# Optimization experiments

Measured on AMD Instinct MI355X. Metric: run time of the kernel, lower is better.

Reference implementation:

```python
import jax, jax.numpy as jnp
import numpy as np

EPS = 1e-05


def setup_inputs() -> dict:
    key = jax.random.key(0)
    k1, k2 = jax.random.split(key)
    shape = (4, 1, 192, 192, 192)  # [B, C=1, D, H, W]
    y_pred = jax.random.normal(k1, shape, dtype=jnp.float32)
    y_true = jax.random.normal(k2, shape, dtype=jnp.float32)
    return {"y_pred": y_pred, "y_true": y_true}


def reference(y_pred, y_true):
    # ones-filter conv is exactly a global sum over channel+spatial dims.
    Ii, Ji = y_true, y_pred
    axes = tuple(range(1, Ii.ndim))  # sum over C, D, H, W -> per-batch scalar
    win_size = jnp.asarray(np.prod(Ii.shape[2:]), dtype=Ii.dtype)

    I_sum = jnp.sum(Ii, axis=axes)
    J_sum = jnp.sum(Ji, axis=axes)
    I2_sum = jnp.sum(Ii * Ii, axis=axes)
    J2_sum = jnp.sum(Ji * Ji, axis=axes)
    IJ_sum = jnp.sum(Ii * Ji, axis=axes)

    u_I = I_sum / win_size
    u_J = J_sum / win_size

    cross = IJ_sum - u_J * I_sum - u_I * J_sum + u_I * u_J * win_size
    I_var = I2_sum - 2 * u_I * I_sum + u_I * u_I * win_size
    J_var = J2_sum - 2 * u_J * J_sum + u_J * u_J * win_size

    cc = cross / (jnp.sqrt(I_var) * jnp.sqrt(J_var) + EPS)  # [B]
    # original: reshape to [B, 1] then mean over dim 1 -> [B]
    return cc
```

## Files before the change

### kernel.cpp

```cpp
#include <hip/hip_runtime.h>
#include <math.h>

#define EPS 1e-05

static constexpr int BLOCK  = 256;
static constexpr int BPB    = 768;
static constexpr int KPT    = 9;
static constexpr int NBATCH = 4;
static constexpr long long NPB = 192LL * 192LL * 192LL;

typedef float v4f __attribute__((ext_vector_type(4)));

__device__ __forceinline__ double wave_reduce(double v) {
    #pragma unroll
    for (int off = 32; off > 0; off >>= 1)
        v += __shfl_down(v, off, 64);
    return v;
}

__global__ __launch_bounds__(BLOCK, 4) void ncc_partial(
    const float* __restrict__ y_pred, const float* __restrict__ y_true,
    double* __restrict__ part)
{
    const int b  = blockIdx.y;
    const int bx = blockIdx.x;
    const v4f* __restrict__ I4 = (const v4f*)(y_true + (long long)b * NPB);
    const v4f* __restrict__ J4 = (const v4f*)(y_pred + (long long)b * NPB);

    const unsigned base = (unsigned)bx * (BLOCK * KPT) + threadIdx.x;

    v4f vI  = {0.f, 0.f, 0.f, 0.f};
    v4f vJ  = {0.f, 0.f, 0.f, 0.f};
    v4f vI2 = {0.f, 0.f, 0.f, 0.f};
    v4f vJ2 = {0.f, 0.f, 0.f, 0.f};
    v4f vIJ = {0.f, 0.f, 0.f, 0.f};

    #pragma unroll
    for (int k = 0; k < KPT; ++k) {
        v4f a = I4[base + k * BLOCK];
        v4f c = J4[base + k * BLOCK];
        vI  += a;
        vJ  += c;
        vI2 += a * a;
        vJ2 += c * c;
        vIJ += a * c;
    }

    double sI  = ((double)vI.x  + (double)vI.y)  + ((double)vI.z  + (double)vI.w);
    double sJ  = ((double)vJ.x  + (double)vJ.y)  + ((double)vJ.z  + (double)vJ.w);
    double sI2 = ((double)vI2.x + (double)vI2.y) + ((double)vI2.z + (double)vI2.w);
    double sJ2 = ((double)vJ2.x + (double)vJ2.y) + ((double)vJ2.z + (double)vJ2.w);
    double sIJ = ((double)vIJ.x + (double)vIJ.y) + ((double)vIJ.z + (double)vIJ.w);

    sI  = wave_reduce(sI);
    sJ  = wave_reduce(sJ);
    sI2 = wave_reduce(sI2);
    sJ2 = wave_reduce(sJ2);
    sIJ = wave_reduce(sIJ);

    __shared__ double lds[BLOCK / 64][5];
    const int wave = threadIdx.x >> 6;
    const int lane = threadIdx.x & 63;
    if (lane == 0) {
        lds[wave][0] = sI;  lds[wave][1] = sJ;
        lds[wave][2] = sI2; lds[wave][3] = sJ2;
        lds[wave][4] = sIJ;
    }
    __syncthreads();
    if (threadIdx.x == 0) {
        double* p = part + ((long long)b * BPB + bx) * 5;
        #pragma unroll
        for (int k = 0; k < 5; ++k)
            p[k] = ((lds[0][k] + lds[1][k]) + (lds[2][k] + lds[3][k]));
    }
}

__global__ __launch_bounds__(BLOCK) void ncc_final(
    const double* __restrict__ part, float* __restrict__ out)
{
    const int b = blockIdx.x;
    double s[5] = {0.0, 0.0, 0.0, 0.0, 0.0};
    #pragma unroll
    for (int j = 0; j < BPB / BLOCK; ++j) {
        const double* p = part + ((long long)b * BPB + j * BLOCK + threadIdx.x) * 5;
        #pragma unroll
        for (int k = 0; k < 5; ++k) s[k] += p[k];
    }
    #pragma unroll
    for (int k = 0; k < 5; ++k) s[k] = wave_reduce(s[k]);

    __shared__ double lds[BLOCK / 64][5];
    const int wave = threadIdx.x >> 6;
    const int lane = threadIdx.x & 63;
    if (lane == 0) {
        #pragma unroll
        for (int k = 0; k < 5; ++k) lds[wave][k] = s[k];
    }
    __syncthreads();
    if (threadIdx.x == 0) {
        double I_sum  = (lds[0][0] + lds[1][0]) + (lds[2][0] + lds[3][0]);
        double J_sum  = (lds[0][1] + lds[1][1]) + (lds[2][1] + lds[3][1]);
        double I2_sum = (lds[0][2] + lds[1][2]) + (lds[2][2] + lds[3][2]);
        double J2_sum = (lds[0][3] + lds[1][3]) + (lds[2][3] + lds[3][3]);
        double IJ_sum = (lds[0][4] + lds[1][4]) + (lds[2][4] + lds[3][4]);

        const double win = (double)NPB;
        const double u_I = I_sum / win;
        const double u_J = J_sum / win;
        const double cross = IJ_sum - u_J * I_sum - u_I * J_sum + u_I * u_J * win;
        const double I_var = I2_sum - 2.0 * u_I * I_sum + u_I * u_I * win;
        const double J_var = J2_sum - 2.0 * u_J * J_sum + u_J * u_J * win;
        const double cc = cross / (sqrt(I_var) * sqrt(J_var) + EPS);
        out[b] = (float)cc;
    }
}

extern "C" void kernel_launch(void* const* d_in, const int* in_sizes, int n_in,
                              void* d_out, int out_size, void* d_ws, size_t ws_size,
                              hipStream_t stream) {
    const float* y_pred = (const float*)d_in[0];
    const float* y_true = (const float*)d_in[1];
    float* out = (float*)d_out;
    double* part = (double*)d_ws;

    dim3 grid1(BPB, NBATCH);
    ncc_partial<<<grid1, BLOCK, 0, stream>>>(y_pred, y_true, part);
    ncc_final<<<NBATCH, BLOCK, 0, stream>>>(part, out);
}
```

Before: 239.4 us.

## Stream inputs through LDS with global_load_lds multi-buffered pipeline

Replaces direct vector global loads with asynchronous global-to-LDS transfers (global_load_lds) in a 4-deep ring buffer. Each block now processes 27 tiles instead of 9, which cuts the grid from 768 to 256 blocks per batch and simplifies the final reduction. The aim is to keep more bytes in flight per wave and overlap loads with accumulation. In exchange it adds LDS traffic and manual waitcnt handling, and with fewer blocks there may be too little parallelism to hide latency.

```diff
diff --git a/kernel.cpp b/kernel.cpp
--- a/kernel.cpp
+++ b/kernel.cpp
@@ -1,13 +1,17 @@
 #include <hip/hip_runtime.h>
 #include <math.h>
+#include <utility>
 
 #define EPS 1e-05
 
 static constexpr int BLOCK  = 256;
-static constexpr int BPB    = 768;
-static constexpr int KPT    = 9;
+static constexpr int BPB    = 256;
+static constexpr int DEPTH  = 4;
+static constexpr int TILES  = 27;
 static constexpr int NBATCH = 4;
 static constexpr long long NPB = 192LL * 192LL * 192LL;
+static constexpr int TILE_BYTES  = BLOCK * 16;
+static constexpr int BLOCK_BYTES = TILES * TILE_BYTES;
 
 typedef float v4f __attribute__((ext_vector_type(4)));
 
@@ -18,16 +22,70 @@
     return v;
 }
 
-__global__ __launch_bounds__(BLOCK, 4) void ncc_partial(
+__device__ __forceinline__ void stage(const void* g, void* l) {
+    __builtin_amdgcn_global_load_lds((const unsigned int*)g, (unsigned int*)l,
+                                     16, 0, 2);
+}
+
+template <int T>
+__device__ __forceinline__ void tile_step(
+    const char* bI, const char* bJ,
+    v4f (*lI)[BLOCK], v4f (*lJ)[BLOCK],
+    unsigned tid, unsigned wave,
+    v4f& vI, v4f& vJ, v4f& vI2, v4f& vJ2, v4f& vIJ)
+{
+    constexpr int rem  = TILES - 1 - T;
+    constexpr int WAIT = (2 * rem < 2 * (DEPTH - 1)) ? 2 * rem : 2 * (DEPTH - 1);
+    asm volatile("s_waitcnt vmcnt(%0)" :: "i"(WAIT) : "memory");
+
+    constexpr int d = T % DEPTH;
+    v4f a = lI[d][tid];
+    v4f c = lJ[d][tid];
+    vI  += a;
+    vJ  += c;
+    vI2 += a * a;
+    vJ2 += c * c;
+    vIJ += a * c;
+
+    if constexpr (T + DEPTH < TILES) {
+        asm volatile("s_waitcnt lgkmcnt(0)" ::: "memory");
+        stage(bI + (T + DEPTH) * TILE_BYTES + tid * 16, &lI[d][wave << 6]);
+        stage(bJ + (T + DEPTH) * TILE_BYTES + tid * 16, &lJ[d][wave << 6]);
+    }
+}
+
+template <int... Ts>
+__device__ __forceinline__ void run_tiles(
+    std::integer_sequence<int, Ts...>,
+    const char* bI, const char* bJ,
+    v4f (*lI)[BLOCK], v4f (*lJ)[BLOCK],
+    unsigned tid, unsigned wave,
+    v4f& vI, v4f& vJ, v4f& vI2, v4f& vJ2, v4f& vIJ)
+{
+    (tile_step<Ts>(bI, bJ, lI, lJ, tid, wave, vI, vJ, vI2, vJ2, vIJ), ...);
+}
+
+__global__ __launch_bounds__(BLOCK) void ncc_partial(
     const float* __restrict__ y_pred, const float* __restrict__ y_true,
     double* __restrict__ part)
 {
+    __shared__ v4f ldsI[DEPTH][BLOCK];
+    __shared__ v4f ldsJ[DEPTH][BLOCK];
+    __shared__ double red[BLOCK / 64][5];
+
     const int b  = blockIdx.y;
     const int bx = blockIdx.x;
-    const v4f* __restrict__ I4 = (const v4f*)(y_true + (long long)b * NPB);
-    const v4f* __restrict__ J4 = (const v4f*)(y_pred + (long long)b * NPB);
+    const unsigned tid  = threadIdx.x;
+    const unsigned wave = tid >> 6;
 
-    const unsigned base = (unsigned)bx * (BLOCK * KPT) + threadIdx.x;
+    const char* bI = (const char*)(y_true + (long long)b * NPB) + (long long)bx * BLOCK_BYTES;
+    const char* bJ = (const char*)(y_pred + (long long)b * NPB) + (long long)bx * BLOCK_BYTES;
+
+    #pragma unroll
+    for (int d = 0; d < DEPTH; ++d) {
+        stage(bI + d * TILE_BYTES + tid * 16, &ldsI[d][wave << 6]);
+        stage(bJ + d * TILE_BYTES + tid * 16, &ldsJ[d][wave << 6]);
+    }
 
     v4f vI  = {0.f, 0.f, 0.f, 0.f};
     v4f vJ  = {0.f, 0.f, 0.f, 0.f};
@@ -35,16 +93,8 @@
     v4f vJ2 = {0.f, 0.f, 0.f, 0.f};
     v4f vIJ = {0.f, 0.f, 0.f, 0.f};
 
-    #pragma unroll
-    for (int k = 0; k < KPT; ++k) {
-        v4f a = I4[base + k * BLOCK];
-        v4f c = J4[base + k * BLOCK];
-        vI  += a;
-        vJ  += c;
-        vI2 += a * a;
-        vJ2 += c * c;
-        vIJ += a * c;
-    }
+    run_tiles(std::make_integer_sequence<int, TILES>{},
+              bI, bJ, ldsI, ldsJ, tid, wave, vI, vJ, vI2, vJ2, vIJ);
 
     double sI  = ((double)vI.x  + (double)vI.y)  + ((double)vI.z  + (double)vI.w);
     double sJ  = ((double)vJ.x  + (double)vJ.y)  + ((double)vJ.z  + (double)vJ.w);
@@ -58,20 +108,18 @@
     sJ2 = wave_reduce(sJ2);
     sIJ = wave_reduce(sIJ);
 
-    __shared__ double lds[BLOCK / 64][5];
-    const int wave = threadIdx.x >> 6;
-    const int lane = threadIdx.x & 63;
+    const int lane = tid & 63;
     if (lane == 0) {
-        lds[wave][0] = sI;  lds[wave][1] = sJ;
-        lds[wave][2] = sI2; lds[wave][3] = sJ2;
-        lds[wave][4] = sIJ;
+        red[wave][0] = sI;  red[wave][1] = sJ;
+        red[wave][2] = sI2; red[wave][3] = sJ2;
+        red[wave][4] = sIJ;
     }
     __syncthreads();
-    if (threadIdx.x == 0) {
+    if (tid == 0) {
         double* p = part + ((long long)b * BPB + bx) * 5;
         #pragma unroll
         for (int k = 0; k < 5; ++k)
-            p[k] = ((lds[0][k] + lds[1][k]) + (lds[2][k] + lds[3][k]));
+            p[k] = ((red[0][k] + red[1][k]) + (red[2][k] + red[3][k]));
     }
 }
 
@@ -79,13 +127,10 @@
     const double* __restrict__ part, float* __restrict__ out)
 {
     const int b = blockIdx.x;
-    double s[5] = {0.0, 0.0, 0.0, 0.0, 0.0};
+    const double* p = part + ((long long)b * BPB + threadIdx.x) * 5;
+    double s[5];
     #pragma unroll
-    for (int j = 0; j < BPB / BLOCK; ++j) {
-        const double* p = part + ((long long)b * BPB + j * BLOCK + threadIdx.x) * 5;
-        #pragma unroll
-        for (int k = 0; k < 5; ++k) s[k] += p[k];
-    }
+    for (int k = 0; k < 5; ++k) s[k] = p[k];
     #pragma unroll
     for (int k = 0; k < 5; ++k) s[k] = wave_reduce(s[k]);
 
```

Result: faster. 216.2 us (-9.7%).
